# Optimization experiments

Hardware: AMD Instinct MI355X
Metric: run time of the kernel (lower is better)

Reference implementation:

```python
import jax, jax.numpy as jnp
import numpy as np

WORLD_SIZE = 8
M_LOCAL = 1024  # max_M // world_size
K = 4096
N = 4096


def setup_inputs() -> dict:
    key = jax.random.key(0)
    k1, k2 = jax.random.split(key)
    # per-rank input shards; all-gather concatenates them along M
    input_shards = jax.random.normal(k1, (WORLD_SIZE, M_LOCAL, K), dtype=jnp.float32)
    # weight stored [N, K] (transed_weight=False path: weight.shape[1] == K)
    weight = jax.random.normal(k2, (N, K), dtype=jnp.float32) * 0.02
    return {"input_shards": input_shards, "weight": weight, "transed_weight": 0}


def reference(input_shards, weight, transed_weight):
    # All-gather across ranks along M: concat shards -> [max_M, K]
    gathered = input_shards.reshape(-1, input_shards.shape[-1])
    # GEMM: out[m, n] = sum_k gathered[m, k] * W[k, n]
    w_kn = weight if transed_weight else weight.T  # -> [K, N]
    return jnp.einsum("mk,kn->mn", gathered, w_kn)
```

## Files before the change

### kernel.cpp

```cpp
#include <hip/hip_runtime.h>
#include <hip/hip_bf16.h>
#include <stdint.h>

#define K_DIM 4096
#define N_DIM 4096
#define BM 256
#define BN 128

typedef short short8 __attribute__((ext_vector_type(8)));
typedef float f32x4 __attribute__((ext_vector_type(4)));
typedef unsigned short ushort_t;
typedef unsigned short ushort8 __attribute__((ext_vector_type(8)));

__device__ __forceinline__ ushort_t f2bf(float f) {
    uint32_t u = __float_as_uint(f);
    u += 0x7FFFu + ((u >> 16) & 1u);
    return (ushort_t)(u >> 16);
}

__global__ void cast_to_bf16_2(const float* __restrict__ a, const float* __restrict__ w,
                               ushort_t* __restrict__ out_a, ushort_t* __restrict__ out_w,
                               int n8a, int n8w) {
    int i = blockIdx.x * blockDim.x + threadIdx.x;
    const float* in;
    ushort_t* out;
    int j;
    if (i < n8a) { in = a; out = out_a; j = i; }
    else if (i < n8a + n8w) { in = w; out = out_w; j = i - n8a; }
    else return;
    const float4* p = (const float4*)in + (size_t)j * 2;
    float4 v0 = p[0];
    float4 v1 = p[1];
    ushort8 r;
    r[0] = f2bf(v0.x); r[1] = f2bf(v0.y); r[2] = f2bf(v0.z); r[3] = f2bf(v0.w);
    r[4] = f2bf(v1.x); r[5] = f2bf(v1.y); r[6] = f2bf(v1.z); r[7] = f2bf(v1.w);
    *((ushort8*)out + j) = r;
}

__global__ __launch_bounds__(512) void gemm_bf16_bt(
    const ushort_t* __restrict__ A,
    const ushort_t* __restrict__ B,
    float* __restrict__ C)
{
    __shared__ ushort_t lds_a[BM * 32];
    __shared__ ushort_t lds_b[BN * 32];

    const int pid   = blockIdx.x;
    const int pid_n = pid & (N_DIM / BN - 1);
    const int pid_m = pid >> 5;
    const int tile_m = pid_m * BM;
    const int tile_n = pid_n * BN;

    const int lane = threadIdx.x & 63;
    const int wave = threadIdx.x >> 6;
    const int wm = (wave >> 1) * 64;
    const int wn = (wave & 1) * 64;
    const int row16 = lane & 15;
    const int quad  = lane >> 4;
    const int ksw   = quad ^ ((row16 >> 1) & 3);

    f32x4 acc[4][4] = {};

    for (int k0 = 0; k0 < K_DIM; k0 += 32) {
        #pragma unroll
        for (int i = 0; i < 3; ++i) {
            int cbase = wave * 192 + i * 64;
            int c     = cbase + lane;
            if (cbase < 1024) {
                int row = c >> 2;
                int kch = (c & 3) ^ ((row >> 1) & 3);
                const ushort_t* ga = A + (size_t)(tile_m + row) * K_DIM + k0 + kch * 8;
                __builtin_amdgcn_global_load_lds(
                    (const __attribute__((address_space(1))) void*)ga,
                    (__attribute__((address_space(3))) void*)(lds_a + cbase * 8), 16, 0, 0);
            } else {
                int cb  = c - 1024;
                int row = cb >> 2;
                int kch = (cb & 3) ^ ((row >> 1) & 3);
                const ushort_t* gb = B + (size_t)(tile_n + row) * K_DIM + k0 + kch * 8;
                __builtin_amdgcn_global_load_lds(
                    (const __attribute__((address_space(1))) void*)gb,
                    (__attribute__((address_space(3))) void*)(lds_b + (cbase - 1024) * 8), 16, 0, 0);
            }
        }
        __syncthreads();

        short8 a_frag[4], b_frag[4];
        #pragma unroll
        for (int t = 0; t < 4; ++t) {
            a_frag[t] = *(const short8*)(lds_a + (wm + t * 16 + row16) * 32 + ksw * 8);
            b_frag[t] = *(const short8*)(lds_b + (wn + t * 16 + row16) * 32 + ksw * 8);
        }
        #pragma unroll
        for (int mi = 0; mi < 4; ++mi)
            #pragma unroll
            for (int ni = 0; ni < 4; ++ni)
                acc[mi][ni] = __builtin_amdgcn_mfma_f32_16x16x32_bf16(
                    a_frag[mi], b_frag[ni], acc[mi][ni], 0, 0, 0);

        __syncthreads();
    }

    #pragma unroll
    for (int mi = 0; mi < 4; ++mi) {
        #pragma unroll
        for (int r = 0; r < 4; ++r) {
            int m = tile_m + wm + mi * 16 + quad * 4 + r;
            float* crow = C + (size_t)m * N_DIM + tile_n + wn;
            #pragma unroll
            for (int ni = 0; ni < 4; ++ni)
                crow[ni * 16 + row16] = acc[mi][ni][r];
        }
    }
}

__global__ void gemm_naive_f32(const float* __restrict__ A, const float* __restrict__ W,
                               float* __restrict__ C, int m_tot) {
    int n = blockIdx.x * blockDim.x + threadIdx.x;
    int m = blockIdx.y;
    if (n >= N_DIM || m >= m_tot) return;
    const float* a = A + (size_t)m * K_DIM;
    const float* w = W + (size_t)n * K_DIM;
    float s = 0.f;
    for (int k = 0; k < K_DIM; ++k) s += a[k] * w[k];
    C[(size_t)m * N_DIM + n] = s;
}

extern "C" void kernel_launch(void* const* d_in, const int* in_sizes, int n_in,
                              void* d_out, int out_size, void* d_ws, size_t ws_size,
                              hipStream_t stream) {
    const float* a_f32 = (const float*)d_in[0];
    const float* w_f32 = (const float*)d_in[1];
    float* out = (float*)d_out;

    const size_t a_elems = (size_t)in_sizes[0];
    const size_t w_elems = (size_t)in_sizes[1];
    const int m_tot = (int)(a_elems / K_DIM);

    const size_t need = (a_elems + w_elems) * sizeof(ushort_t);
    if (ws_size >= need && (m_tot % BM) == 0) {
        ushort_t* a_bf = (ushort_t*)d_ws;
        ushort_t* w_bf = a_bf + a_elems;

        int n8a = (int)(a_elems / 8);
        int n8w = (int)(w_elems / 8);
        int n8 = n8a + n8w;
        cast_to_bf16_2<<<(n8 + 255) / 256, 256, 0, stream>>>(a_f32, w_f32, a_bf, w_bf, n8a, n8w);

        int nblocks = (N_DIM / BN) * (m_tot / BM);
        gemm_bf16_bt<<<nblocks, 512, 0, stream>>>(a_bf, w_bf, out);
    } else {
        dim3 grid(N_DIM / 256, m_tot);
        gemm_naive_f32<<<grid, 256, 0, stream>>>(a_f32, w_f32, out, m_tot);
    }
}
```

Before: 538.9 us.

## Rewrite bf16 GEMM as 256x256-tile multi-stage pipelined kernel with grid swizzle

Replaces the single-buffered 256x128 GEMM, which synchronises twice per 32-wide K step, with a 256x256 tile kernel. It uses four LDS K-slices (two 64-wide K tiles, each split into two 32-wide halves) and an eight-phase software pipeline that interleaves global-to-LDS loads with MFMA work under explicit vmcnt waits and barriers. It also remaps block IDs across eight groups to improve L2 reuse, and raises MFMA priority with setprio. The aim is to hide global load latency and raise arithmetic intensity per tile. In exchange it uses more registers (32 accumulators per thread) and 128 KB of LDS per block, and depends on hand-tuned wait counts for correctness.

After: 499.8 us. 1.08x faster.

```diff
diff --git a/kernel.cpp b/kernel.cpp
--- a/kernel.cpp
+++ b/kernel.cpp
@@ -1,11 +1,12 @@
 #include <hip/hip_runtime.h>
-#include <hip/hip_bf16.h>
 #include <stdint.h>
 
 #define K_DIM 4096
 #define N_DIM 4096
 #define BM 256
-#define BN 128
+#define BN 256
+#define NTILES (K_DIM / 64)
+#define NIT (NTILES / 2)
 
 typedef short short8 __attribute__((ext_vector_type(8)));
 typedef float f32x4 __attribute__((ext_vector_type(4)));
@@ -37,79 +38,160 @@
     *((ushort8*)out + j) = r;
 }
 
-__global__ __launch_bounds__(512) void gemm_bf16_bt(
+__device__ __forceinline__ void wgbar() {
+    asm volatile("" ::: "memory");
+    __builtin_amdgcn_s_barrier();
+    asm volatile("" ::: "memory");
+}
+
+
+#define LDS_A(b, kk) (sA + ((b) * 2 + (kk)) * 8192)
+#define LDS_B(b, kk) (sB + ((b) * 2 + (kk)) * 8192)
+
+#define LOAD_AF(af, b, kk, mih) { _Pragma("unroll") for (int t = 0; t < 4; ++t) { \
+    int row = wm + (mih) * 64 + t * 16 + row16;                                   \
+    af[t] = *(const short8*)(LDS_A(b, kk) + row * 32 + ksw * 8); } }
+
+#define LOAD_BF(bfr, b, kk) { _Pragma("unroll") for (int t = 0; t < 4; ++t) {     \
+    int row = wn + t * 16 + row16;                                                \
+    bfr[t] = *(const short8*)(LDS_B(b, kk) + row * 32 + ksw * 8); } }
+
+#define MFMA16(mih, af, bfr) { __builtin_amdgcn_s_setprio(1);                     \
+    _Pragma("unroll") for (int t = 0; t < 4; ++t)                                 \
+    _Pragma("unroll") for (int n = 0; n < 4; ++n)                                 \
+        acc[(mih) * 4 + t][n] = __builtin_amdgcn_mfma_f32_16x16x32_bf16(          \
+            af[t], bfr[n], acc[(mih) * 4 + t][n], 0, 0, 0);                       \
+    __builtin_amdgcn_s_setprio(0); }
+
+#define LGKM0() asm volatile("s_waitcnt lgkmcnt(0)")
+#define VMCNT4() asm volatile("s_waitcnt vmcnt(4)" ::: "memory")
+
+__global__ __launch_bounds__(512, 2) void gemm_bf16_8ph(
     const ushort_t* __restrict__ A,
     const ushort_t* __restrict__ B,
     float* __restrict__ C)
 {
-    __shared__ ushort_t lds_a[BM * 32];
-    __shared__ ushort_t lds_b[BN * 32];
-
-    const int pid   = blockIdx.x;
-    const int pid_n = pid & (N_DIM / BN - 1);
-    const int pid_m = pid >> 5;
+    __shared__ ushort_t sA[2 * 2 * 8192];
+    __shared__ ushort_t sB[2 * 2 * 8192];
+
+    const int pid0 = blockIdx.x;
+    const int pid  = (pid0 & 7) * (int)(gridDim.x >> 3) + (pid0 >> 3);
+    const int pid_n = pid & 15;
+    const int pid_m = pid >> 4;
     const int tile_m = pid_m * BM;
     const int tile_n = pid_n * BN;
 
-    const int lane = threadIdx.x & 63;
-    const int wave = threadIdx.x >> 6;
-    const int wm = (wave >> 1) * 64;
-    const int wn = (wave & 1) * 64;
+    const int lane  = threadIdx.x & 63;
+    const int wave  = threadIdx.x >> 6;
+    const int wm    = (wave >> 2) * 128;
+    const int wn    = (wave & 3) * 64;
     const int row16 = lane & 15;
     const int quad  = lane >> 4;
     const int ksw   = quad ^ ((row16 >> 1) & 3);
 
-    f32x4 acc[4][4] = {};
-
-    for (int k0 = 0; k0 < K_DIM; k0 += 32) {
+    int cb[2];
+    size_t goff[2];
+    #pragma unroll
+    for (int j = 0; j < 2; ++j) {
+        cb[j] = wave * 64 + j * 512;
+        int c = cb[j] + lane;
+        int r = c >> 2;
+        int q = (c & 3) ^ ((r >> 1) & 3);
+        goff[j] = (size_t)r * K_DIM + q * 8;
+    }
+    const ushort_t* Abase = A + (size_t)tile_m * K_DIM;
+    const ushort_t* Bbase = B + (size_t)tile_n * K_DIM;
+
+    auto STAGE = [&](const ushort_t* gbase, ushort_t* lds, int k0) {
         #pragma unroll
-        for (int i = 0; i < 3; ++i) {
-            int cbase = wave * 192 + i * 64;
-            int c     = cbase + lane;
-            if (cbase < 1024) {
-                int row = c >> 2;
-                int kch = (c & 3) ^ ((row >> 1) & 3);
-                const ushort_t* ga = A + (size_t)(tile_m + row) * K_DIM + k0 + kch * 8;
-                __builtin_amdgcn_global_load_lds(
-                    (const __attribute__((address_space(1))) void*)ga,
-                    (__attribute__((address_space(3))) void*)(lds_a + cbase * 8), 16, 0, 0);
-            } else {
-                int cb  = c - 1024;
-                int row = cb >> 2;
-                int kch = (cb & 3) ^ ((row >> 1) & 3);
-                const ushort_t* gb = B + (size_t)(tile_n + row) * K_DIM + k0 + kch * 8;
-                __builtin_amdgcn_global_load_lds(
-                    (const __attribute__((address_space(1))) void*)gb,
-                    (__attribute__((address_space(3))) void*)(lds_b + (cbase - 1024) * 8), 16, 0, 0);
-            }
+        for (int j = 0; j < 2; ++j) {
+            const ushort_t* gp = gbase + goff[j] + k0;
+            __builtin_amdgcn_global_load_lds(
+                (const __attribute__((address_space(1))) void*)gp,
+                (__attribute__((address_space(3))) void*)(lds + cb[j] * 8), 16, 0, 0);
         }
-        __syncthreads();
-
-        short8 a_frag[4], b_frag[4];
-        #pragma unroll
-        for (int t = 0; t < 4; ++t) {
-            a_frag[t] = *(const short8*)(lds_a + (wm + t * 16 + row16) * 32 + ksw * 8);
-            b_frag[t] = *(const short8*)(lds_b + (wn + t * 16 + row16) * 32 + ksw * 8);
-        }
-        #pragma unroll
-        for (int mi = 0; mi < 4; ++mi)
-            #pragma unroll
-            for (int ni = 0; ni < 4; ++ni)
-                acc[mi][ni] = __builtin_amdgcn_mfma_f32_16x16x32_bf16(
-                    a_frag[mi], b_frag[ni], acc[mi][ni], 0, 0, 0);
-
-        __syncthreads();
+    };
+
+    f32x4 acc[8][4] = {};
+
+    STAGE(Abase, LDS_A(0, 0), 0);
+    STAGE(Bbase, LDS_B(0, 0), 0);
+    STAGE(Abase, LDS_A(0, 1), 32);
+    STAGE(Bbase, LDS_B(0, 1), 32);
+    STAGE(Abase, LDS_A(1, 0), 64);
+    STAGE(Bbase, LDS_B(1, 0), 64);
+    VMCNT4();
+    wgbar();
+
+    short8 af[4], bfr[4];
+
+    #pragma unroll 1
+    for (int i = 0; i < NIT; ++i) {
+        const int k1 = (2 * i + 1) * 64;
+        int t2 = 2 * i + 2; if (t2 > NTILES - 1) t2 = NTILES - 1;
+        int t3 = 2 * i + 3; if (t3 > NTILES - 1) t3 = NTILES - 1;
+        const int k2 = t2 * 64, k3 = t3 * 64;
+
+        LOAD_AF(af, 0, 0, 0); LOAD_BF(bfr, 0, 0);
+        STAGE(Abase, LDS_A(1, 1), k1 + 32);
+        wgbar(); LGKM0();
+        MFMA16(0, af, bfr);
+        wgbar();
+
+        LOAD_AF(af, 0, 0, 1);
+        STAGE(Bbase, LDS_B(1, 1), k1 + 32);
+        wgbar(); LGKM0();
+        MFMA16(1, af, bfr);
+        wgbar();
+
+        LOAD_AF(af, 0, 1, 0); LOAD_BF(bfr, 0, 1);
+        STAGE(Abase, LDS_A(0, 0), k2);
+        wgbar(); LGKM0();
+        MFMA16(0, af, bfr);
+        wgbar();
+
+        LOAD_AF(af, 0, 1, 1);
+        STAGE(Bbase, LDS_B(0, 0), k2);
+        VMCNT4();
+        wgbar(); LGKM0();
+        MFMA16(1, af, bfr);
+        wgbar();
+
+        LOAD_AF(af, 1, 0, 0); LOAD_BF(bfr, 1, 0);
+        STAGE(Abase, LDS_A(0, 1), k2 + 32);
+        wgbar(); LGKM0();
+        MFMA16(0, af, bfr);
+        wgbar();
+
+        LOAD_AF(af, 1, 0, 1);
+        STAGE(Bbase, LDS_B(0, 1), k2 + 32);
+        wgbar(); LGKM0();
+        MFMA16(1, af, bfr);
+        wgbar();
+
+        LOAD_AF(af, 1, 1, 0); LOAD_BF(bfr, 1, 1);
+        STAGE(Abase, LDS_A(1, 0), k3);
+        wgbar(); LGKM0();
+        MFMA16(0, af, bfr);
+        wgbar();
+
+        LOAD_AF(af, 1, 1, 1);
+        STAGE(Bbase, LDS_B(1, 0), k3);
+        VMCNT4();
+        wgbar(); LGKM0();
+        MFMA16(1, af, bfr);
+        wgbar();
     }
 
     #pragma unroll
-    for (int mi = 0; mi < 4; ++mi) {
+    for (int mi = 0; mi < 8; ++mi) {
         #pragma unroll
         for (int r = 0; r < 4; ++r) {
             int m = tile_m + wm + mi * 16 + quad * 4 + r;
             float* crow = C + (size_t)m * N_DIM + tile_n + wn;
             #pragma unroll
-            for (int ni = 0; ni < 4; ++ni)
-                crow[ni * 16 + row16] = acc[mi][ni][r];
+            for (int n = 0; n < 4; ++n)
+                crow[n * 16 + row16] = acc[mi][n][r];
         }
     }
 }
@@ -138,7 +220,7 @@
     const int m_tot = (int)(a_elems / K_DIM);
 
     const size_t need = (a_elems + w_elems) * sizeof(ushort_t);
-    if (ws_size >= need && (m_tot % BM) == 0) {
+    if (ws_size >= need && (m_tot % BM) == 0 && w_elems == (size_t)N_DIM * K_DIM) {
         ushort_t* a_bf = (ushort_t*)d_ws;
         ushort_t* w_bf = a_bf + a_elems;
 
@@ -148,7 +230,7 @@
         cast_to_bf16_2<<<(n8 + 255) / 256, 256, 0, stream>>>(a_f32, w_f32, a_bf, w_bf, n8a, n8w);
 
         int nblocks = (N_DIM / BN) * (m_tot / BM);
-        gemm_bf16_bt<<<nblocks, 512, 0, stream>>>(a_bf, w_bf, out);
+        gemm_bf16_8ph<<<nblocks, 512, 0, stream>>>(a_bf, w_bf, out);
     } else {
         dim3 grid(N_DIM / 256, m_tot);
         gemm_naive_f32<<<grid, 256, 0, stream>>>(a_f32, w_f32, out, m_tot);
```
